# Performance work log

Measured on AMD Instinct MI355X. Metric: run time of the kernel, lower is better.

Reference implementation:

```python
import jax, jax.numpy as jnp
import numpy as np

N = 8192        # number of nodes (dense adjacency)
IN_DIM = 128    # GCN in_dim
OUT_DIM = 128   # GCN out_dim
MASK_THRESH = 0.8
NEG_INF = 1e9


def setup_inputs() -> dict:
    key = jax.random.key(0)
    kA, kX, kW = jax.random.split(key, 3)
    A = jax.random.uniform(kA, (N, N), dtype=jnp.float32)
    X = jax.random.normal(kX, (N, IN_DIM), dtype=jnp.float32)
    # nn.Linear(in_dim, out_dim): weight [out_dim, in_dim], bias [out_dim]
    W = jax.random.normal(kW, (OUT_DIM, IN_DIM), dtype=jnp.float32) * (1.0 / np.sqrt(IN_DIM))
    b = jnp.zeros((OUT_DIM,), dtype=jnp.float32)
    return {"A": A, "X": X, "W": W, "b": b}


def reference(A, X, W, b):
    # GCN.forward: A_norm = softmax(A - 1e9 * (A <= 0.8), axis=-1)
    # out = leaky_relu(A_norm @ Linear(X))   (relu=True path)
    logits = A - NEG_INF * (A <= MASK_THRESH).astype(A.dtype)   # [N, N]
    A_norm = jax.nn.softmax(logits, axis=-1)                     # row-wise softmax
    XW = X @ W.T + b                                             # [N, OUT_DIM]
    return jax.nn.leaky_relu(A_norm @ XW, negative_slope=0.01)   # [N, OUT_DIM]
```

## Files before the change

kernel.cpp:

```cpp
#include <hip/hip_runtime.h>
#include <hip/hip_bf16.h>

#define N_NODES 8192
#define DIM 128
#define MASK_THRESH 0.8f
#define RB 64
#define KSTEP 64

using f32x4  = __attribute__((ext_vector_type(4))) float;
using bf16x8 = __attribute__((ext_vector_type(8))) short;

static __device__ __forceinline__ short f2bf(float f) {
    unsigned u = __builtin_bit_cast(unsigned, f);
    u += 0x7fffu + ((u >> 16) & 1u);
    return (short)(u >> 16);
}

static __device__ __forceinline__ void gload16(const void* gsrc, void* ldst) {
    __builtin_amdgcn_global_load_lds(
        (const __attribute__((address_space(1))) unsigned int*)gsrc,
        (__attribute__((address_space(3))) unsigned int*)ldst,
        16, 0, 0);
}

__global__ __launch_bounds__(256) void build_vf_kernel(
    const float* __restrict__ X, const float* __restrict__ W,
    const float* __restrict__ bias, short* __restrict__ Vf) {
    __shared__ float xs[32][128];
    const int jt = blockIdx.x * 32;
    for (int e = threadIdx.x; e < 32 * 128; e += 256) {
        xs[e >> 7][e & 127] = X[(size_t)(jt + (e >> 7)) * DIM + (e & 127)];
    }
    __syncthreads();
    const int d  = threadIdx.x & 127;
    const int jh = threadIdx.x >> 7;
    float bv = bias[d];
    float acc[16];
#pragma unroll
    for (int i = 0; i < 16; i++) acc[i] = bv;
    const float* wrow = W + (size_t)d * DIM;
    for (int k = 0; k < DIM; k += 4) {
        f32x4 wv = *(const f32x4*)(wrow + k);
#pragma unroll
        for (int i = 0; i < 16; i++) {
            f32x4 xv = *(const f32x4*)(&xs[jh * 16 + i][k]);
            acc[i] = fmaf(xv[0], wv[0], acc[i]);
            acc[i] = fmaf(xv[1], wv[1], acc[i]);
            acc[i] = fmaf(xv[2], wv[2], acc[i]);
            acc[i] = fmaf(xv[3], wv[3], acc[i]);
        }
    }
    bf16x8 o0, o1;
#pragma unroll
    for (int i = 0; i < 8; i++) { o0[i] = f2bf(acc[i]); o1[i] = f2bf(acc[8 + i]); }
    const int kb = jt >> 5;
    const int t  = d >> 4;
    short* base = Vf + ((size_t)(kb * 8 + t) * 64 + (d & 15) + 32 * jh) * 8;
    *(bf16x8*)(base)       = o0;
    *(bf16x8*)(base + 128) = o1;
}

template <int WRITE_PARTIAL>
__global__ __launch_bounds__(256, 2) void fused_kernel(
    const float* __restrict__ A, const short* __restrict__ Vf,
    float* __restrict__ dst, float* __restrict__ Zp, int kchunk) {

    __shared__ __align__(16) float abuf[16384];
    __shared__ float zs[2][64];

    const int tid   = threadIdx.x;
    const int wid   = tid >> 6;
    const int lane  = tid & 63;
    const int row_a = lane & 15;
    const int kg    = lane >> 4;
    const int wr    = wid & 1;
    const int wc    = wid >> 1;
    const int rb    = blockIdx.x & (RB - 1);
    const int chunk = blockIdx.x >> 6;
    const int r0    = rb * 128;
    const int k0    = chunk * kchunk;
    const int nsteps = kchunk >> 6;

    f32x4 acc[4][4];
#pragma unroll
    for (int rg = 0; rg < 4; rg++)
#pragma unroll
        for (int t = 0; t < 4; t++) acc[rg][t] = (f32x4)0.0f;
    float zacc[4] = {0.0f, 0.0f, 0.0f, 0.0f};

    const int sub   = lane >> 4;
    const int schnk = lane & 15;

#pragma unroll
    for (int i = 0; i < 8; i++) {
        const int row_s = wid * 32 + i * 4 + sub;
        gload16(A + (size_t)(r0 + row_s) * N_NODES + k0 + ((schnk ^ (row_s & 15)) << 2),
                abuf + (wid * 32 + i * 4) * 64);
    }

    for (int ks = 0; ks < nsteps; ks++) {
        __syncthreads();
        if (ks + 1 < nsteps) {
            float* nb = abuf + ((ks + 1) & 1) * 8192;
#pragma unroll
            for (int i = 0; i < 8; i++) {
                const int row_s = wid * 32 + i * 4 + sub;
                gload16(A + (size_t)(r0 + row_s) * N_NODES + k0 + (ks + 1) * KSTEP
                          + ((schnk ^ (row_s & 15)) << 2),
                        nb + (wid * 32 + i * 4) * 64);
            }
        }
        const float* ab = abuf + (ks & 1) * 8192;
        const int kb_glob = (k0 >> 5) + ks * 2;
#pragma unroll
        for (int kb = 0; kb < 2; kb++) {
            bf16x8 bv[4];
#pragma unroll
            for (int t = 0; t < 4; t++)
                bv[t] = *(const bf16x8*)(Vf + ((size_t)(kb_glob + kb) * 8 + wc * 4 + t) * 512 + lane * 8);
#pragma unroll
            for (int rg = 0; rg < 4; rg++) {
                const int row  = wr * 64 + rg * 16 + row_a;
                const int base = row * 64;
                const int c0   = kb * 8 + kg * 2;
                const f32x4 av0 = *(const f32x4*)(ab + base + (((c0 + 0) ^ row_a) << 2));
                const f32x4 av1 = *(const f32x4*)(ab + base + (((c0 + 1) ^ row_a) << 2));
                float p[8];
#pragma unroll
                for (int i = 0; i < 4; i++) {
                    p[i]     = (av0[i] > MASK_THRESH) ? __expf(av0[i]) : 0.0f;
                    p[i + 4] = (av1[i] > MASK_THRESH) ? __expf(av1[i]) : 0.0f;
                }
                bf16x8 af;
#pragma unroll
                for (int i = 0; i < 8; i++) { zacc[rg] += p[i]; af[i] = f2bf(p[i]); }
#pragma unroll
                for (int t = 0; t < 4; t++)
                    acc[rg][t] = __builtin_amdgcn_mfma_f32_16x16x32_bf16(af, bv[t], acc[rg][t], 0, 0, 0);
            }
        }
    }

#pragma unroll
    for (int rg = 0; rg < 4; rg++) {
        zacc[rg] += __shfl_xor(zacc[rg], 16);
        zacc[rg] += __shfl_xor(zacc[rg], 32);
    }
    if (wc == 0 && lane < 16) {
#pragma unroll
        for (int rg = 0; rg < 4; rg++) zs[wr][rg * 16 + lane] = zacc[rg];
    }
    __syncthreads();

    if (WRITE_PARTIAL) {
        float* nd = dst + (size_t)chunk * N_NODES * DIM;
#pragma unroll
        for (int rg = 0; rg < 4; rg++)
#pragma unroll
            for (int t = 0; t < 4; t++)
#pragma unroll
                for (int r = 0; r < 4; r++) {
                    const int row = r0 + wr * 64 + rg * 16 + kg * 4 + r;
                    const int col = wc * 64 + t * 16 + row_a;
                    nd[(size_t)row * DIM + col] = acc[rg][t][r];
                }
        if (wc == 0 && lane < 16) {
#pragma unroll
            for (int rg = 0; rg < 4; rg++)
                Zp[(size_t)chunk * N_NODES + r0 + wr * 64 + rg * 16 + lane] = zacc[rg];
        }
    } else {
#pragma unroll
        for (int rg = 0; rg < 4; rg++)
#pragma unroll
            for (int t = 0; t < 4; t++)
#pragma unroll
                for (int r = 0; r < 4; r++) {
                    const int row = r0 + wr * 64 + rg * 16 + kg * 4 + r;
                    const int col = wc * 64 + t * 16 + row_a;
                    const float v = acc[rg][t][r] / zs[wr][rg * 16 + kg * 4 + r];
                    dst[(size_t)row * DIM + col] = (v > 0.0f) ? v : 0.01f * v;
                }
    }
}

__global__ __launch_bounds__(256) void reduce_kernel(
    const float* __restrict__ num, const float* __restrict__ Zp,
    float* __restrict__ out, int S) {
    const size_t i4 = (size_t)blockIdx.x * 256 + threadIdx.x;
    const int r  = (int)(i4 >> 5);
    const int c4 = (int)(i4 & 31) * 4;
    f32x4 s = (f32x4)0.0f;
    float z = 0.0f;
    for (int p = 0; p < S; p++) {
        s += *(const f32x4*)(num + ((size_t)p * N_NODES + r) * DIM + c4);
        z += Zp[(size_t)p * N_NODES + r];
    }
    f32x4 o;
#pragma unroll
    for (int j = 0; j < 4; j++) {
        const float v = s[j] / z;
        o[j] = (v > 0.0f) ? v : 0.01f * v;
    }
    *(f32x4*)(out + (size_t)r * DIM + c4) = o;
}

extern "C" void kernel_launch(void* const* d_in, const int* in_sizes, int n_in,
                              void* d_out, int out_size, void* d_ws, size_t ws_size,
                              hipStream_t stream) {
    const float* A = (const float*)d_in[0];
    const float* X = (const float*)d_in[1];
    const float* W = (const float*)d_in[2];
    const float* b = (const float*)d_in[3];
    float* out = (float*)d_out;

    const size_t VF_BYTES = (size_t)DIM * N_NODES * 2;
    short* Vf = (short*)d_ws;
    build_vf_kernel<<<N_NODES / 32, 256, 0, stream>>>(X, W, b, Vf);

    const size_t per_split = ((size_t)N_NODES * DIM + N_NODES) * sizeof(float);
    int S = 1;
    for (int cand = 8; cand >= 1; cand >>= 1) {
        if (VF_BYTES + (size_t)cand * per_split <= ws_size) { S = cand; break; }
    }

    if (S >= 2) {
        float* num = (float*)((char*)d_ws + VF_BYTES);
        float* Zp  = num + (size_t)S * N_NODES * DIM;
        fused_kernel<1><<<RB * S, 256, 0, stream>>>(A, Vf, num, Zp, N_NODES / S);
        reduce_kernel<<<(N_NODES * DIM / 4) / 256, 256, 0, stream>>>(num, Zp, out, S);
    } else {
        fused_kernel<0><<<RB, 256, 0, stream>>>(A, Vf, out, nullptr, N_NODES);
    }
}
```

Before: 125.8 us.

## Shrink fused tile to 64 rows for higher occupancy and more blocks

```diff
diff --git a/kernel.cpp b/kernel.cpp
--- a/kernel.cpp
+++ b/kernel.cpp
@@ -4,7 +4,7 @@
 #define N_NODES 8192
 #define DIM 128
 #define MASK_THRESH 0.8f
-#define RB 64
+#define RB 128
 #define KSTEP 64
 
 using f32x4  = __attribute__((ext_vector_type(4))) float;
@@ -61,12 +61,11 @@
 }
 
 template <int WRITE_PARTIAL>
-__global__ __launch_bounds__(256, 2) void fused_kernel(
+__global__ __launch_bounds__(256, 5) void fused_kernel(
     const float* __restrict__ A, const short* __restrict__ Vf,
-    float* __restrict__ dst, float* __restrict__ Zp, int kchunk) {
-
-    __shared__ __align__(16) float abuf[16384];
-    __shared__ float zs[2][64];
+    float* __restrict__ dst, float* __restrict__ Zp, int kchunk, int S) {
+
+    __shared__ __align__(16) float abuf[8192];
 
     const int tid   = threadIdx.x;
     const int wid   = tid >> 6;
@@ -75,56 +74,53 @@
     const int kg    = lane >> 4;
     const int wr    = wid & 1;
     const int wc    = wid >> 1;
-    const int rb    = blockIdx.x & (RB - 1);
-    const int chunk = blockIdx.x >> 6;
-    const int r0    = rb * 128;
+    const int rb    = blockIdx.x / S;
+    const int chunk = blockIdx.x - rb * S;
+    const int r0    = rb * 64;
     const int k0    = chunk * kchunk;
     const int nsteps = kchunk >> 6;
 
-    f32x4 acc[4][4];
-#pragma unroll
-    for (int rg = 0; rg < 4; rg++)
+    f32x4 acc[2][4];
+#pragma unroll
+    for (int rg = 0; rg < 2; rg++)
 #pragma unroll
         for (int t = 0; t < 4; t++) acc[rg][t] = (f32x4)0.0f;
-    float zacc[4] = {0.0f, 0.0f, 0.0f, 0.0f};
-
-    const int sub   = lane >> 4;
-    const int schnk = lane & 15;
-
-#pragma unroll
-    for (int i = 0; i < 8; i++) {
-        const int row_s = wid * 32 + i * 4 + sub;
-        gload16(A + (size_t)(r0 + row_s) * N_NODES + k0 + ((schnk ^ (row_s & 15)) << 2),
-                abuf + (wid * 32 + i * 4) * 64);
-    }
+    float zacc[2] = {0.0f, 0.0f};
+
+    const float* asrc[4]; int adst[4];
+#pragma unroll
+    for (int i = 0; i < 4; i++) {
+        const int row_s = wid * 16 + i * 4 + (lane >> 4);
+        asrc[i] = A + (size_t)(r0 + row_s) * N_NODES + k0
+                    + (((lane & 15) ^ (row_s & 7)) << 2);
+        adst[i] = (wid * 16 + i * 4) * 64;
+    }
+
+#pragma unroll
+    for (int i = 0; i < 4; i++) gload16(asrc[i], abuf + adst[i]);
 
     for (int ks = 0; ks < nsteps; ks++) {
         __syncthreads();
         if (ks + 1 < nsteps) {
-            float* nb = abuf + ((ks + 1) & 1) * 8192;
-#pragma unroll
-            for (int i = 0; i < 8; i++) {
-                const int row_s = wid * 32 + i * 4 + sub;
-                gload16(A + (size_t)(r0 + row_s) * N_NODES + k0 + (ks + 1) * KSTEP
-                          + ((schnk ^ (row_s & 15)) << 2),
-                        nb + (wid * 32 + i * 4) * 64);
-            }
-        }
-        const float* ab = abuf + (ks & 1) * 8192;
-        const int kb_glob = (k0 >> 5) + ks * 2;
+            float* nb = abuf + ((ks + 1) & 1) * 4096;
+#pragma unroll
+            for (int i = 0; i < 4; i++)
+                gload16(asrc[i] + (size_t)(ks + 1) * KSTEP, nb + adst[i]);
+        }
+        const float* ab = abuf + (ks & 1) * 4096;
+        const int kbg = (k0 >> 5) + ks * 2;
 #pragma unroll
         for (int kb = 0; kb < 2; kb++) {
             bf16x8 bv[4];
 #pragma unroll
             for (int t = 0; t < 4; t++)
-                bv[t] = *(const bf16x8*)(Vf + ((size_t)(kb_glob + kb) * 8 + wc * 4 + t) * 512 + lane * 8);
-#pragma unroll
-            for (int rg = 0; rg < 4; rg++) {
-                const int row  = wr * 64 + rg * 16 + row_a;
-                const int base = row * 64;
+                bv[t] = *(const bf16x8*)(Vf + ((size_t)(kbg + kb) * 8 + wc * 4 + t) * 512 + lane * 8);
+#pragma unroll
+            for (int rg = 0; rg < 2; rg++) {
+                const int base = (wr * 32 + rg * 16 + row_a) * 64;
                 const int c0   = kb * 8 + kg * 2;
-                const f32x4 av0 = *(const f32x4*)(ab + base + (((c0 + 0) ^ row_a) << 2));
-                const f32x4 av1 = *(const f32x4*)(ab + base + (((c0 + 1) ^ row_a) << 2));
+                const f32x4 av0 = *(const f32x4*)(ab + base + (((c0 + 0) ^ (row_a & 7)) << 2));
+                const f32x4 av1 = *(const f32x4*)(ab + base + (((c0 + 1) ^ (row_a & 7)) << 2));
                 float p[8];
 #pragma unroll
                 for (int i = 0; i < 4; i++) {
@@ -142,44 +138,46 @@
     }
 
 #pragma unroll
-    for (int rg = 0; rg < 4; rg++) {
+    for (int rg = 0; rg < 2; rg++) {
         zacc[rg] += __shfl_xor(zacc[rg], 16);
         zacc[rg] += __shfl_xor(zacc[rg], 32);
     }
-    if (wc == 0 && lane < 16) {
-#pragma unroll
-        for (int rg = 0; rg < 4; rg++) zs[wr][rg * 16 + lane] = zacc[rg];
-    }
-    __syncthreads();
 
     if (WRITE_PARTIAL) {
         float* nd = dst + (size_t)chunk * N_NODES * DIM;
 #pragma unroll
-        for (int rg = 0; rg < 4; rg++)
+        for (int rg = 0; rg < 2; rg++)
 #pragma unroll
             for (int t = 0; t < 4; t++)
 #pragma unroll
                 for (int r = 0; r < 4; r++) {
-                    const int row = r0 + wr * 64 + rg * 16 + kg * 4 + r;
+                    const int row = r0 + wr * 32 + rg * 16 + kg * 4 + r;
                     const int col = wc * 64 + t * 16 + row_a;
                     nd[(size_t)row * DIM + col] = acc[rg][t][r];
                 }
         if (wc == 0 && lane < 16) {
 #pragma unroll
-            for (int rg = 0; rg < 4; rg++)
-                Zp[(size_t)chunk * N_NODES + r0 + wr * 64 + rg * 16 + lane] = zacc[rg];
+            for (int rg = 0; rg < 2; rg++)
+                Zp[(size_t)chunk * N_NODES + r0 + wr * 32 + rg * 16 + lane] = zacc[rg];
         }
     } else {
-#pragma unroll
-        for (int rg = 0; rg < 4; rg++)
+        __syncthreads();
+        float* zsm = abuf;
+        if (wc == 0 && lane < 16) {
+            zsm[wr * 32 + lane]      = zacc[0];
+            zsm[wr * 32 + 16 + lane] = zacc[1];
+        }
+        __syncthreads();
+#pragma unroll
+        for (int rg = 0; rg < 2; rg++)
 #pragma unroll
             for (int t = 0; t < 4; t++)
 #pragma unroll
                 for (int r = 0; r < 4; r++) {
-                    const int row = r0 + wr * 64 + rg * 16 + kg * 4 + r;
+                    const int rl  = wr * 32 + rg * 16 + kg * 4 + r;
                     const int col = wc * 64 + t * 16 + row_a;
-                    const float v = acc[rg][t][r] / zs[wr][rg * 16 + kg * 4 + r];
-                    dst[(size_t)row * DIM + col] = (v > 0.0f) ? v : 0.01f * v;
+                    const float v = acc[rg][t][r] / zsm[rl];
+                    dst[(size_t)(r0 + rl) * DIM + col] = (v > 0.0f) ? v : 0.01f * v;
                 }
     }
 }
@@ -227,9 +225,9 @@
     if (S >= 2) {
         float* num = (float*)((char*)d_ws + VF_BYTES);
         float* Zp  = num + (size_t)S * N_NODES * DIM;
-        fused_kernel<1><<<RB * S, 256, 0, stream>>>(A, Vf, num, Zp, N_NODES / S);
+        fused_kernel<1><<<RB * S, 256, 0, stream>>>(A, Vf, num, Zp, N_NODES / S, S);
         reduce_kernel<<<(N_NODES * DIM / 4) / 256, 256, 0, stream>>>(num, Zp, out, S);
     } else {
-        fused_kernel<0><<<RB, 256, 0, stream>>>(A, Vf, out, nullptr, N_NODES);
-    }
-}
+        fused_kernel<0><<<RB, 256, 0, stream>>>(A, Vf, out, nullptr, N_NODES, 1);
+    }
+}
```

Measured after the change: 160.5 us. 27.6% more time.
